# Kernel tuning notes

Hardware: AMD Instinct MI355X
Metric: run time of the kernel (lower is better)

Reference implementation:

```python
import jax, jax.numpy as jnp
import numpy as np

SEQ, B, I, H, O = 2048, 128, 64, 256, 64


def setup_inputs() -> dict:
    key = jax.random.key(0)
    ks = jax.random.split(key, 7)
    s_ih = 1.0 / np.sqrt(I)
    s_hh = 1.0 / np.sqrt(H)
    return {
        "x": jax.random.normal(ks[0], (SEQ, B, I), dtype=jnp.float32),
        "h0": jnp.zeros((B, H), dtype=jnp.float32),
        "c0": jnp.zeros((B, H), dtype=jnp.float32),
        "W_ih": jax.random.uniform(ks[1], (4 * H, I), minval=-s_ih, maxval=s_ih, dtype=jnp.float32),
        "W_hh": jax.random.uniform(ks[2], (4 * H, H), minval=-s_hh, maxval=s_hh, dtype=jnp.float32),
        "b": jax.random.uniform(ks[3], (4 * H,), minval=-s_hh, maxval=s_hh, dtype=jnp.float32),
        "W_out": jax.random.uniform(ks[4], (O, H), minval=-s_hh, maxval=s_hh, dtype=jnp.float32),
        "b_out": jax.random.uniform(ks[5], (O,), minval=-s_hh, maxval=s_hh, dtype=jnp.float32),
    }


def reference(x, h0, c0, W_ih, W_hh, b, W_out, b_out):
    # Precompute input-to-hidden projection for all timesteps in one big GEMM:
    # (SEQ, B, I) @ (I, 4H) -> (SEQ, B, 4H)
    xW = jnp.einsum("sbi,gi->sbg", x, W_ih) + b

    def step(carry, xw_t):
        h, c = carry
        lin = xw_t + h @ W_hh.T  # (B, 4H); eqx gate order i, f, g, o
        i_g, f_g, g_g, o_g = jnp.split(lin, 4, axis=-1)
        i_g = jax.nn.sigmoid(i_g)
        f_g = jax.nn.sigmoid(f_g)
        g_g = jnp.tanh(g_g)
        o_g = jax.nn.sigmoid(o_g)
        c_new = f_g * c + i_g * g_g
        h_new = o_g * jnp.tanh(c_new)
        return (h_new, c_new), h_new

    _, hs = jax.lax.scan(step, (h0, c0), xW)  # hs: (SEQ, B, H)
    # Linear readout applied per (seq, batch) position
    return jnp.einsum("sbh,oh->sbo", hs, W_out) + b_out
```

## Files before the change

### kernel.cpp

```cpp
#include <hip/hip_runtime.h>
#include <cstdint>

#define SEQ   2048
#define BATCH 128
#define IN    64
#define HID   256
#define OUTD  64

#define T     512
#define NHH   32
#define NIH   8

#define OFF_WHH  0
#define SZ_WHH   (2*NHH*512*4)
#define OFF_WIH  (OFF_WHH+SZ_WHH)
#define SZ_WIH   (2*NIH*512*4)
#define OFF_WOUT (OFF_WIH+SZ_WIH)
#define SZ_WOUT  8192
#define OFF_EXCH (OFF_WOUT+SZ_WOUT)
#define SZ_EXCH  (BATCH*2*2*512)
#define OFF_FLAG (OFF_EXCH+SZ_EXCH)
#define SZ_FLAG  (BATCH*2*16)
#define TOTAL_DW (OFF_FLAG+SZ_FLAG)

typedef _Float16 f16x2 __attribute__((ext_vector_type(2)));

__device__ __forceinline__ float fexp2(float v) { return __builtin_amdgcn_exp2f(v); }
__device__ __forceinline__ float frcp(float v)  { return __builtin_amdgcn_rcpf(v); }
__device__ __forceinline__ float fsig(float v)  { return frcp(1.0f + fexp2(v * -1.44269504088896f)); }
__device__ __forceinline__ float ftanh_(float v){ return 1.0f - 2.0f * frcp(1.0f + fexp2(v * 2.88539008177793f)); }

__device__ __forceinline__ unsigned int pack2d(float a, float b) {
  unsigned short lo = __builtin_bit_cast(unsigned short, (_Float16)a);
  unsigned short hi = __builtin_bit_cast(unsigned short, (_Float16)b);
  return (unsigned int)lo | ((unsigned int)hi << 16);
}

__device__ __forceinline__ float dot2f(unsigned int w, unsigned int h, float acc) {
#if __has_builtin(__builtin_amdgcn_fdot2)
  return __builtin_amdgcn_fdot2(__builtin_bit_cast(f16x2, w), __builtin_bit_cast(f16x2, h), acc, false);
#else
  f16x2 a = __builtin_bit_cast(f16x2, w), b = __builtin_bit_cast(f16x2, h);
  return acc + (float)a.x * (float)b.x + (float)a.y * (float)b.y;
#endif
}

__device__ __forceinline__ void mac8(uint4 w, uint4 h, float& acc) {
  acc = dot2f(w.x, h.x, acc);
  acc = dot2f(w.y, h.y, acc);
  acc = dot2f(w.z, h.z, acc);
  acc = dot2f(w.w, h.w, acc);
}

__global__ void prep_weights(const float* __restrict__ Whh, const float* __restrict__ Wih,
                             const float* __restrict__ Wout, unsigned int* __restrict__ ws) {
  int tid = blockIdx.x * 256 + threadIdx.x;
  if (tid >= TOTAL_DW) return;
  if (tid >= OFF_FLAG) { ws[tid] = 0u; return; }
  if (tid >= OFF_EXCH) return;
  unsigned int val;
  if (tid < OFF_WIH) {
    int q = tid & 3, t = (tid >> 2) & 511, rest = tid >> 11;
    int j = rest & 31, half = rest >> 5;
    const float* p = Whh + (size_t)(half*512 + t)*HID + 8*j + 2*q;
    val = pack2d(p[0], p[1]);
  } else if (tid < OFF_WOUT) {
    int r = tid - OFF_WIH;
    int q = r & 3, t = (r >> 2) & 511, rest = r >> 11;
    int j = rest & 7, half = rest >> 3;
    const float* p = Wih + (size_t)(half*512 + t)*IN + 8*j + 2*q;
    val = pack2d(p[0], p[1]);
  } else {
    int r = tid - OFF_WOUT;
    const float* p = Wout + 2*r;
    val = pack2d(p[0], p[1]);
  }
  ws[tid] = val;
}

__global__ __launch_bounds__(512, 2) void lstm_main(
    const float* __restrict__ x, const float* __restrict__ h0, const float* __restrict__ c0,
    const float* __restrict__ bias, const float* __restrict__ b_out,
    unsigned int* __restrict__ ws, float* __restrict__ out)
{
  const int bid = blockIdx.x;
  const int b = bid >> 1, half = bid & 1, t = threadIdx.x;

  __shared__ __align__(16) unsigned char smem[86016];
  float*          lin_sh = (float*)smem;
  unsigned short* hs     = (unsigned short*)(smem + 2048);
  unsigned short* hs2    = (unsigned short*)(smem + 2560);
  unsigned short* xs     = (unsigned short*)(smem + 3328);

  const unsigned int* WhhS = ws + OFF_WHH;
  const unsigned int* WihS = ws + OFF_WIH;
  const unsigned short* WoutS = (const unsigned short*)(ws + OFF_WOUT);
  float* exch = (float*)(ws + OFF_EXCH);
  float* ebuf_my   = exch + (size_t)bid      * 1024;
  float* ebuf_peer = exch + (size_t)(bid ^ 1)* 1024;
  unsigned int* flagv = ws + OFF_FLAG;
  unsigned int* myflag = flagv + (size_t)bid * 16;
  unsigned int* pflag  = flagv + (size_t)(bid ^ 1) * 16;

  uint4 whh[NHH];
  #pragma unroll
  for (int j = 0; j < NHH; ++j)
    whh[j] = *(const uint4*)(WhhS + ((size_t)(half*NHH + j)*512 + t)*4);
  uint4 wih[NIH];
  #pragma unroll
  for (int j = 0; j < NIH; ++j)
    wih[j] = *(const uint4*)(WihS + ((size_t)(half*NIH + j)*512 + t)*4);
  const int oglob = half*32 + (t >> 4), seg = t & 15;
  uint4 wo[2];
  #pragma unroll
  for (int q = 0; q < 2; ++q)
    wo[q] = *(const uint4*)(WoutS + (size_t)oglob*256 + seg*16 + q*8);

  float c = 0.0f;
  if (t < HID) {
    c = c0[(size_t)b*HID + t];
    unsigned short hv0 = (unsigned short)(pack2d(h0[(size_t)b*HID + t], 0.0f) & 0xffffu);
    hs[t] = hv0;
    hs2[(t >> 4)*24 + (t & 15)] = hv0;
  } else if (t < HID + 32) {
    int i = t - HID;
    float2 xx = *(const float2*)(x + (size_t)b*IN + 2*i);
    ((unsigned int*)xs)[i] = pack2d(xx.x, xx.y);
  }
  const float bz = bias[half*512 + t];
  const float bo = b_out[oglob];
  __syncthreads();

  for (int s = 0; s < SEQ; ++s) {
    float2 xn = make_float2(0.0f, 0.0f);
    if (t >= HID && t < HID + 32) {
      int sn = (s + 1 < SEQ) ? s + 1 : s;
      xn = *(const float2*)(x + ((size_t)sn*BATCH + b)*IN + 2*(t - HID));
    }

    float la = bz, lb = 0.0f;
    #pragma unroll
    for (int j = 0; j < NHH; j += 2) {
      uint4 h0v = *(const uint4*)(hs + 8*j);
      uint4 h1v = *(const uint4*)(hs + 8*j + 8);
      mac8(whh[j],   h0v, la);
      mac8(whh[j+1], h1v, lb);
    }
    #pragma unroll
    for (int j = 0; j < NIH; j += 2) {
      uint4 x0v = *(const uint4*)(xs + 8*j);
      uint4 x1v = *(const uint4*)(xs + 8*j + 8);
      mac8(wih[j],   x0v, la);
      mac8(wih[j+1], x1v, lb);
    }
    float lin = la + lb;
    lin_sh[t] = lin;
    __hip_atomic_store(ebuf_my + (s & 1)*512 + t, lin,
                       __ATOMIC_RELAXED, __HIP_MEMORY_SCOPE_AGENT);

    __syncthreads();

    if (t == 0)
      __hip_atomic_store(myflag, (unsigned)(s + 1),
                         __ATOMIC_RELAXED, __HIP_MEMORY_SCOPE_AGENT);

    if (t < HID) {
      float own_a = lin_sh[t];
      float own_b = lin_sh[t + 256];
      while (__hip_atomic_load(pflag, __ATOMIC_RELAXED, __HIP_MEMORY_SCOPE_AGENT) <= (unsigned)s) {}
      __asm__ volatile("" ::: "memory");
      float* pb = ebuf_peer + (s & 1)*512;
      float p_a = __hip_atomic_load(pb + t,       __ATOMIC_RELAXED, __HIP_MEMORY_SCOPE_AGENT);
      float p_b = __hip_atomic_load(pb + t + 256, __ATOMIC_RELAXED, __HIP_MEMORY_SCOPE_AGENT);
      float li, lf, lg, lo_;
      if (half == 0) { li = own_a; lf = own_b; lg = p_a;  lo_ = p_b; }
      else           { lg = own_a; lo_ = own_b; li = p_a; lf  = p_b; }
      float ig = fsig(li), fg = fsig(lf), gg = ftanh_(lg), og = fsig(lo_);
      c = fg*c + ig*gg;
      float hn = og*ftanh_(c);
      unsigned short hp = (unsigned short)(pack2d(hn, 0.0f) & 0xffffu);
      hs[t] = hp;
      hs2[(t >> 4)*24 + (t & 15)] = hp;
    } else if (t < HID + 32) {
      ((unsigned int*)xs)[t - HID] = pack2d(xn.x, xn.y);
    }
    __syncthreads();

    float acc = 0.0f;
    #pragma unroll
    for (int q = 0; q < 2; ++q) {
      uint4 hv = *(const uint4*)(hs2 + seg*24 + 8*q);
      mac8(wo[q], hv, acc);
    }
    acc += __shfl_xor(acc, 1);
    acc += __shfl_xor(acc, 2);
    acc += __shfl_xor(acc, 4);
    acc += __shfl_xor(acc, 8);
    if (seg == 0) out[((size_t)s*BATCH + b)*OUTD + oglob] = acc + bo;
  }
}

extern "C" void kernel_launch(void* const* d_in, const int* in_sizes, int n_in,
                              void* d_out, int out_size, void* d_ws, size_t ws_size,
                              hipStream_t stream) {
  const float* x     = (const float*)d_in[0];
  const float* h0    = (const float*)d_in[1];
  const float* c0    = (const float*)d_in[2];
  const float* W_ih  = (const float*)d_in[3];
  const float* W_hh  = (const float*)d_in[4];
  const float* bias  = (const float*)d_in[5];
  const float* W_out = (const float*)d_in[6];
  const float* b_out = (const float*)d_in[7];
  float* out = (float*)d_out;
  unsigned int* ws = (unsigned int*)d_ws;

  hipLaunchKernelGGL(prep_weights, dim3((TOTAL_DW + 255)/256), dim3(256), 0, stream,
                     W_hh, W_ih, W_out, ws);
  hipLaunchKernelGGL(lstm_main, dim3(2*BATCH), dim3(T), 0, stream,
                     x, h0, c0, bias, b_out, ws, out);
}
```

Measured before the change: 5.338 ms.

## Split LSTM by hidden units and exchange h halves instead of gate pre-activations

The hidden dimension is now split across the block pair, and each block owns all four gates for 128 hidden units, so gate nonlinearities need no peer data. Each step exchanges the fp16 halves of h (256 bytes) through global memory instead of 512 fp32 gate pre-activations. The exchange is overlapped with the own-half recurrent matmul, and the output projection is deferred by one step to share barriers. Block pairing moves from adjacent to bid^128, and register pinning of the weights is added. The cost is an extra barrier per step and a spin-wait that now sits on the critical path before the peer-half matmul.

```diff
diff --git a/kernel.cpp b/kernel.cpp
--- a/kernel.cpp
+++ b/kernel.cpp
@@ -18,9 +18,9 @@
 #define OFF_WOUT (OFF_WIH+SZ_WIH)
 #define SZ_WOUT  8192
 #define OFF_EXCH (OFF_WOUT+SZ_WOUT)
-#define SZ_EXCH  (BATCH*2*2*512)
+#define SZ_EXCH  (2*BATCH*2*64)
 #define OFF_FLAG (OFF_EXCH+SZ_EXCH)
-#define SZ_FLAG  (BATCH*2*16)
+#define SZ_FLAG  (2*BATCH*16)
 #define TOTAL_DW (OFF_FLAG+SZ_FLAG)
 
 typedef _Float16 f16x2 __attribute__((ext_vector_type(2)));
@@ -51,6 +51,8 @@
   acc = dot2f(w.z, h.z, acc);
   acc = dot2f(w.w, h.w, acc);
 }
+
+#define PIN4(v) asm volatile("" : "+v"((v).x), "+v"((v).y), "+v"((v).z), "+v"((v).w))
 
 __global__ void prep_weights(const float* __restrict__ Whh, const float* __restrict__ Wih,
                              const float* __restrict__ Wout, unsigned int* __restrict__ ws) {
@@ -61,14 +63,17 @@
   unsigned int val;
   if (tid < OFF_WIH) {
     int q = tid & 3, t = (tid >> 2) & 511, rest = tid >> 11;
-    int j = rest & 31, half = rest >> 5;
-    const float* p = Whh + (size_t)(half*512 + t)*HID + 8*j + 2*q;
+    int slot = rest & 31, half = rest >> 5;
+    int c = (half*16 + slot) & 31;
+    int row = (t >> 7)*256 + half*128 + (t & 127);
+    const float* p = Whh + (size_t)row*HID + 8*c + 2*q;
     val = pack2d(p[0], p[1]);
   } else if (tid < OFF_WOUT) {
     int r = tid - OFF_WIH;
     int q = r & 3, t = (r >> 2) & 511, rest = r >> 11;
     int j = rest & 7, half = rest >> 3;
-    const float* p = Wih + (size_t)(half*512 + t)*IN + 8*j + 2*q;
+    int row = (t >> 7)*256 + half*128 + (t & 127);
+    const float* p = Wih + (size_t)row*IN + 8*j + 2*q;
     val = pack2d(p[0], p[1]);
   } else {
     int r = tid - OFF_WOUT;
@@ -84,120 +89,145 @@
     unsigned int* __restrict__ ws, float* __restrict__ out)
 {
   const int bid = blockIdx.x;
-  const int b = bid >> 1, half = bid & 1, t = threadIdx.x;
-
-  __shared__ __align__(16) unsigned char smem[86016];
-  float*          lin_sh = (float*)smem;
-  unsigned short* hs     = (unsigned short*)(smem + 2048);
-  unsigned short* hs2    = (unsigned short*)(smem + 2560);
-  unsigned short* xs     = (unsigned short*)(smem + 3328);
+  const int b = bid & 127, half = bid >> 7, t = threadIdx.x;
+  const int base_own = half*128, base_peer = 128 - half*128;
+
+  __shared__ __align__(16) float lin_sh[T];
+  __shared__ __align__(16) unsigned short hs[HID];
+  __shared__ __align__(16) unsigned short xs[IN];
 
   const unsigned int* WhhS = ws + OFF_WHH;
   const unsigned int* WihS = ws + OFF_WIH;
   const unsigned short* WoutS = (const unsigned short*)(ws + OFF_WOUT);
-  float* exch = (float*)(ws + OFF_EXCH);
-  float* ebuf_my   = exch + (size_t)bid      * 1024;
-  float* ebuf_peer = exch + (size_t)(bid ^ 1)* 1024;
-  unsigned int* flagv = ws + OFF_FLAG;
+  unsigned short* E = (unsigned short*)(ws + OFF_EXCH);
+  unsigned short* myE = E + (size_t)bid * 256;
+  const unsigned short* peerE = E + (size_t)(bid ^ 128) * 256;
+  unsigned int* flagv  = ws + OFF_FLAG;
   unsigned int* myflag = flagv + (size_t)bid * 16;
-  unsigned int* pflag  = flagv + (size_t)(bid ^ 1) * 16;
+  unsigned int* pflag  = flagv + (size_t)(bid ^ 128) * 16;
 
   uint4 whh[NHH];
   #pragma unroll
-  for (int j = 0; j < NHH; ++j)
+  for (int j = 0; j < NHH; ++j) {
     whh[j] = *(const uint4*)(WhhS + ((size_t)(half*NHH + j)*512 + t)*4);
+    PIN4(whh[j]);
+  }
   uint4 wih[NIH];
   #pragma unroll
-  for (int j = 0; j < NIH; ++j)
+  for (int j = 0; j < NIH; ++j) {
     wih[j] = *(const uint4*)(WihS + ((size_t)(half*NIH + j)*512 + t)*4);
+    PIN4(wih[j]);
+  }
   const int oglob = half*32 + (t >> 4), seg = t & 15;
   uint4 wo[2];
   #pragma unroll
-  for (int q = 0; q < 2; ++q)
+  for (int q = 0; q < 2; ++q) {
     wo[q] = *(const uint4*)(WoutS + (size_t)oglob*256 + seg*16 + q*8);
+    PIN4(wo[q]);
+  }
 
   float c = 0.0f;
-  if (t < HID) {
-    c = c0[(size_t)b*HID + t];
-    unsigned short hv0 = (unsigned short)(pack2d(h0[(size_t)b*HID + t], 0.0f) & 0xffffu);
-    hs[t] = hv0;
-    hs2[(t >> 4)*24 + (t & 15)] = hv0;
-  } else if (t < HID + 32) {
-    int i = t - HID;
+  if (t < 128) c = c0[(size_t)b*HID + base_own + t];
+  if (t < 256) {
+    hs[t] = (unsigned short)(pack2d(h0[(size_t)b*HID + t], 0.0f) & 0xffffu);
+  } else if (t < 288) {
+    int i = t - 256;
     float2 xx = *(const float2*)(x + (size_t)b*IN + 2*i);
     ((unsigned int*)xs)[i] = pack2d(xx.x, xx.y);
   }
-  const float bz = bias[half*512 + t];
+  const float bz = bias[(t >> 7)*256 + half*128 + (t & 127)];
   const float bo = b_out[oglob];
   __syncthreads();
 
   for (int s = 0; s < SEQ; ++s) {
+    float la = bz, lb = 0.0f;
+    #pragma unroll
+    for (int k = 0; k < 16; ++k) {
+      uint4 hv = *(const uint4*)(hs + base_own + 8*k);
+      if (k & 1) mac8(whh[k], hv, lb); else mac8(whh[k], hv, la);
+    }
+    #pragma unroll
+    for (int j = 0; j < NIH; ++j) {
+      uint4 xv = *(const uint4*)(xs + 8*j);
+      if (j & 1) mac8(wih[j], xv, lb); else mac8(wih[j], xv, la);
+    }
+
     float2 xn = make_float2(0.0f, 0.0f);
-    if (t >= HID && t < HID + 32) {
+    if (t >= 256 && t < 288) {
       int sn = (s + 1 < SEQ) ? s + 1 : s;
-      xn = *(const float2*)(x + ((size_t)sn*BATCH + b)*IN + 2*(t - HID));
-    }
-
-    float la = bz, lb = 0.0f;
-    #pragma unroll
-    for (int j = 0; j < NHH; j += 2) {
-      uint4 h0v = *(const uint4*)(hs + 8*j);
-      uint4 h1v = *(const uint4*)(hs + 8*j + 8);
-      mac8(whh[j],   h0v, la);
-      mac8(whh[j+1], h1v, lb);
-    }
-    #pragma unroll
-    for (int j = 0; j < NIH; j += 2) {
-      uint4 x0v = *(const uint4*)(xs + 8*j);
-      uint4 x1v = *(const uint4*)(xs + 8*j + 8);
-      mac8(wih[j],   x0v, la);
-      mac8(wih[j+1], x1v, lb);
-    }
-    float lin = la + lb;
-    lin_sh[t] = lin;
-    __hip_atomic_store(ebuf_my + (s & 1)*512 + t, lin,
-                       __ATOMIC_RELAXED, __HIP_MEMORY_SCOPE_AGENT);
-
+      xn = *(const float2*)(x + ((size_t)sn*BATCH + b)*IN + 2*(t - 256));
+    }
+    if (s > 0 && t < 64) {
+      while (__hip_atomic_load(pflag, __ATOMIC_RELAXED, __HIP_MEMORY_SCOPE_AGENT) < (unsigned)s) {}
+      __asm__ volatile("" ::: "memory");
+      unsigned int u = __hip_atomic_load((const unsigned int*)peerE + (s & 1)*64 + t,
+                                         __ATOMIC_RELAXED, __HIP_MEMORY_SCOPE_AGENT);
+      ((unsigned int*)(hs + base_peer))[t] = u;
+    }
     __syncthreads();
 
-    if (t == 0)
-      __hip_atomic_store(myflag, (unsigned)(s + 1),
-                         __ATOMIC_RELAXED, __HIP_MEMORY_SCOPE_AGENT);
-
-    if (t < HID) {
-      float own_a = lin_sh[t];
-      float own_b = lin_sh[t + 256];
-      while (__hip_atomic_load(pflag, __ATOMIC_RELAXED, __HIP_MEMORY_SCOPE_AGENT) <= (unsigned)s) {}
-      __asm__ volatile("" ::: "memory");
-      float* pb = ebuf_peer + (s & 1)*512;
-      float p_a = __hip_atomic_load(pb + t,       __ATOMIC_RELAXED, __HIP_MEMORY_SCOPE_AGENT);
-      float p_b = __hip_atomic_load(pb + t + 256, __ATOMIC_RELAXED, __HIP_MEMORY_SCOPE_AGENT);
-      float li, lf, lg, lo_;
-      if (half == 0) { li = own_a; lf = own_b; lg = p_a;  lo_ = p_b; }
-      else           { lg = own_a; lo_ = own_b; li = p_a; lf  = p_b; }
+    #pragma unroll
+    for (int k = 0; k < 16; ++k) {
+      uint4 hv = *(const uint4*)(hs + base_peer + 8*k);
+      if (k & 1) mac8(whh[16 + k], hv, lb); else mac8(whh[16 + k], hv, la);
+    }
+    lin_sh[t] = la + lb;
+
+    float acc = 0.0f;
+    #pragma unroll
+    for (int q = 0; q < 2; ++q) {
+      uint4 hv = *(const uint4*)(hs + seg*16 + 8*q);
+      mac8(wo[q], hv, acc);
+    }
+    acc += __shfl_xor(acc, 1);
+    acc += __shfl_xor(acc, 2);
+    acc += __shfl_xor(acc, 4);
+    acc += __shfl_xor(acc, 8);
+    if (s > 0 && seg == 0) out[((size_t)(s - 1)*BATCH + b)*OUTD + oglob] = acc + bo;
+
+    __syncthreads();
+
+    if (t < 128) {
+      float li  = lin_sh[t];
+      float lf  = lin_sh[128 + t];
+      float lg  = lin_sh[256 + t];
+      float lo_ = lin_sh[384 + t];
       float ig = fsig(li), fg = fsig(lf), gg = ftanh_(lg), og = fsig(lo_);
       c = fg*c + ig*gg;
       float hn = og*ftanh_(c);
       unsigned short hp = (unsigned short)(pack2d(hn, 0.0f) & 0xffffu);
-      hs[t] = hp;
-      hs2[(t >> 4)*24 + (t & 15)] = hp;
-    } else if (t < HID + 32) {
-      ((unsigned int*)xs)[t - HID] = pack2d(xn.x, xn.y);
+      hs[base_own + t] = hp;
+      __hip_atomic_store(myE + ((s + 1) & 1)*128 + t, hp,
+                         __ATOMIC_RELAXED, __HIP_MEMORY_SCOPE_AGENT);
+    } else if (t >= 256 && t < 288) {
+      ((unsigned int*)xs)[t - 256] = pack2d(xn.x, xn.y);
     }
     __syncthreads();
 
-    float acc = 0.0f;
-    #pragma unroll
-    for (int q = 0; q < 2; ++q) {
-      uint4 hv = *(const uint4*)(hs2 + seg*24 + 8*q);
-      mac8(wo[q], hv, acc);
-    }
-    acc += __shfl_xor(acc, 1);
-    acc += __shfl_xor(acc, 2);
-    acc += __shfl_xor(acc, 4);
-    acc += __shfl_xor(acc, 8);
-    if (seg == 0) out[((size_t)s*BATCH + b)*OUTD + oglob] = acc + bo;
-  }
+    if (t == 0)
+      __hip_atomic_store(myflag, (unsigned)(s + 1),
+                         __ATOMIC_RELAXED, __HIP_MEMORY_SCOPE_AGENT);
+  }
+
+  if (t < 64) {
+    while (__hip_atomic_load(pflag, __ATOMIC_RELAXED, __HIP_MEMORY_SCOPE_AGENT) < (unsigned)SEQ) {}
+    __asm__ volatile("" ::: "memory");
+    unsigned int u = __hip_atomic_load((const unsigned int*)peerE + (SEQ & 1)*64 + t,
+                                       __ATOMIC_RELAXED, __HIP_MEMORY_SCOPE_AGENT);
+    ((unsigned int*)(hs + base_peer))[t] = u;
+  }
+  __syncthreads();
+  float acc = 0.0f;
+  #pragma unroll
+  for (int q = 0; q < 2; ++q) {
+    uint4 hv = *(const uint4*)(hs + seg*16 + 8*q);
+    mac8(wo[q], hv, acc);
+  }
+  acc += __shfl_xor(acc, 1);
+  acc += __shfl_xor(acc, 2);
+  acc += __shfl_xor(acc, 4);
+  acc += __shfl_xor(acc, 8);
+  if (seg == 0) out[((size_t)(SEQ - 1)*BATCH + b)*OUTD + oglob] = acc + bo;
 }
 
 extern "C" void kernel_launch(void* const* d_in, const int* in_sizes, int n_in,
```

New measurement: 7.405 ms. +38.7%, slower.
